# Kernel tuning notes

Measured on AMD Instinct MI355X. Metric: run time of the kernel, lower is better.

The kernel has to match this reference:

```python
import jax, jax.numpy as jnp
import numpy as np


def setup_inputs() -> dict:
    key = jax.random.key(0)
    ks = jax.random.split(key, 24)
    N, C, D_IN, HID, EMB = 8192, 4096, 32, 128, 128
    s = 0.05
    inp = {
        "cand_feat": jax.random.normal(ks[0], (1, C, D_IN), jnp.float32),
        "graph_pos": jax.random.uniform(ks[1], (N, 3), jnp.float32),
        "graph_rad": jax.random.uniform(ks[2], (N,), jnp.float32) + 0.01,
        "L": jnp.ones((1,), jnp.float32),
        "adj": jax.random.uniform(ks[3], (N, N), jnp.float32),
        "mask": jax.random.randint(ks[4], (1, C), 0, 2, jnp.int32),
        # candidate encoder: 32 -> 128 -> 128
        "cW1": jax.random.normal(ks[5], (D_IN, 128), jnp.float32) * s,
        "cb1": jnp.zeros((128,), jnp.float32),
        "cW2": jax.random.normal(ks[6], (128, EMB), jnp.float32) * s,
        "cb2": jnp.zeros((EMB,), jnp.float32),
        # graph encoder input proj: 4 -> 128
        "gW0": jax.random.normal(ks[7], (4, HID), jnp.float32) * s,
        "gb0": jnp.zeros((HID,), jnp.float32),
        # 3 GNN layers: concat(2*HID) -> HID
        "gnnW": jax.random.normal(ks[8], (3, 2 * HID, HID), jnp.float32) * s,
        "gnnb": jnp.zeros((3, HID), jnp.float32),
        # output proj: 2*HID -> EMB
        "goW": jax.random.normal(ks[9], (2 * HID, EMB), jnp.float32) * s,
        "gob": jnp.zeros((EMB,), jnp.float32),
        # fusion: 2*EMB -> 256 -> 128 -> 1
        "fW1": jax.random.normal(ks[10], (2 * EMB, 256), jnp.float32) * s,
        "fb1": jnp.zeros((256,), jnp.float32),
        "fW2": jax.random.normal(ks[11], (256, 128), jnp.float32) * s,
        "fb2": jnp.zeros((128,), jnp.float32),
        "fW3": jax.random.normal(ks[12], (128, 1), jnp.float32) * s,
        "fb3": jnp.zeros((1,), jnp.float32),
    }
    return inp


def reference(cand_feat, graph_pos, graph_rad, L, adj, mask,
              cW1, cb1, cW2, cb2, gW0, gb0, gnnW, gnnb, goW, gob,
              fW1, fb1, fW2, fb2, fW3, fb3):
    relu = jax.nn.relu
    # ---- candidate encoder: [1, C, 32] -> [1, C, 128]
    cand_emb = relu(relu(cand_feat @ cW1 + cb1) @ cW2 + cb2)
    # ---- graph encoder ----
    node = jnp.concatenate([graph_pos / L, (graph_rad / jnp.max(graph_rad))[:, None]], axis=1)  # [N, 4]
    h = relu(node @ gW0 + gb0)  # [N, HID]
    deg = jnp.clip(jnp.sum(adj, axis=-1, keepdims=True), 1.0)  # [N, 1]
    for i in range(gnnW.shape[0]):
        agg = (adj @ h) / deg                       # degree-normalized aggregation
        h = relu(jnp.concatenate([h, agg], axis=-1) @ gnnW[i] + gnnb[i])
    h_glob = jnp.concatenate([jnp.max(h, axis=0), jnp.mean(h, axis=0)], axis=-1)  # [2*HID]
    graph_emb = h_glob @ goW + gob  # [EMB]
    # ---- fusion decoder ----
    g_exp = jnp.broadcast_to(graph_emb[None, None, :], cand_emb.shape)
    combined = jnp.concatenate([cand_emb, g_exp], axis=-1)  # [1, C, 2*EMB]
    scores = (relu(relu(combined @ fW1 + fb1) @ fW2 + fb2) @ fW3 + fb3)[..., 0]  # [1, C]
    return jnp.where(mask == 0, -jnp.inf, scores)
```

## Files before the change

kernel.cpp:

```cpp
#include <hip/hip_runtime.h>
#include <hip/hip_bf16.h>

constexpr int NN  = 8192;
constexpr int CC  = 4096;
constexpr int HD  = 128;
constexpr int KSPLIT = 8;
constexpr int KCHUNK = NN / KSPLIT;
constexpr int NKB = KCHUNK / 32;
constexpr int NK32 = NN / 32;
constexpr int CCH = 32;

typedef __attribute__((ext_vector_type(8))) short bf16x8;
typedef __attribute__((ext_vector_type(4))) float f32x4;

static __device__ __forceinline__ unsigned short f2bf(float f) {
  unsigned int u = __builtin_bit_cast(unsigned int, f);
  unsigned int lsb = (u >> 16) & 1u;
  u += 0x7fffu + lsb;
  return (unsigned short)(u >> 16);
}
static __device__ __forceinline__ float bf2f(unsigned short u) {
  return __builtin_bit_cast(float, ((unsigned int)u) << 16);
}
static __device__ __forceinline__ unsigned long long rfl64(unsigned long long x) {
  unsigned int lo = __builtin_amdgcn_readfirstlane((unsigned int)x);
  unsigned int hi = __builtin_amdgcn_readfirstlane((unsigned int)(x >> 32));
  return ((unsigned long long)hi << 32) | lo;
}

static __device__ __forceinline__ size_t pidx(int t16, int kb, int lane) {
  return (((size_t)t16 * NK32 + kb) * 64 + lane) * 8;
}

__global__ __launch_bounds__(256) void k_radmax(const float* __restrict__ rad, float* out) {
  __shared__ float red[256];
  int t = threadIdx.x;
  float m = 0.0f;
  for (int i = t; i < NN; i += 256) m = fmaxf(m, rad[i]);
  red[t] = m; __syncthreads();
  for (int s = 128; s > 0; s >>= 1) {
    if (t < s) red[t] = fmaxf(red[t], red[t + s]);
    __syncthreads();
  }
  if (t == 0) out[0] = red[0];
}

__global__ __launch_bounds__(256) void k_h0(const float* __restrict__ pos, const float* __restrict__ rad,
                                            const float* __restrict__ Lp, const float* __restrict__ rmax,
                                            const float* __restrict__ gW0, const float* __restrict__ gb0,
                                            float* __restrict__ h, unsigned short* __restrict__ hTP) {
  __shared__ __align__(16) unsigned short lt[128][72];
  int t = threadIdx.x;
  int i0 = blockIdx.x * 64;
  float invL = 1.0f / Lp[0];
  float invR = 1.0f / rmax[0];
  for (int rep = 0; rep < 32; ++rep) {
    int idx = rep * 256 + t;
    int il = idx >> 7, j = idx & 127;
    int i = i0 + il;
    float n0 = pos[i * 3 + 0] * invL, n1 = pos[i * 3 + 1] * invL, n2 = pos[i * 3 + 2] * invL;
    float n3 = rad[i] * invR;
    float v = gb0[j] + n0 * gW0[j] + n1 * gW0[128 + j] + n2 * gW0[256 + j] + n3 * gW0[384 + j];
    v = fmaxf(v, 0.0f);
    h[(size_t)i * HD + j] = v;
    lt[j][il] = f2bf(v);
  }
  __syncthreads();
  #pragma unroll
  for (int it = 0; it < 4; ++it) {
    int idx = it * 256 + t;
    int lane = idx & 63, chunk = idx >> 6;
    int t16 = chunk >> 1, kbL = chunk & 1;
    int j = t16 * 16 + (lane & 15), kg = lane >> 4;
    union { unsigned short v[8]; uint4 q; } pk;
    #pragma unroll
    for (int s = 0; s < 8; ++s) {
      int kp = kg * 4 + (s & 3) + ((s >> 2) * 16);
      pk.v[s] = lt[j][kbL * 32 + kp];
    }
    *(uint4*)(hTP + pidx(t16, blockIdx.x * 2 + kbL, lane)) = pk.q;
  }
}

__global__ __launch_bounds__(256) void k_convP(const float* __restrict__ adj,
                                               unsigned short* __restrict__ adjP,
                                               float* __restrict__ pd) {
  __shared__ __align__(16) unsigned short lt[64 * 256];
  const int t = threadIdx.x;
  const int r0 = blockIdx.x * 64;
  const int c0 = blockIdx.y * 256;
  #pragma unroll
  for (int p = 0; p < 16; ++p) {
    int r = p * 4 + (t >> 6);
    int c = (t & 63) * 4;
    float4 v = *(const float4*)(adj + (size_t)(r0 + r) * NN + c0 + c);
    union { unsigned short u[4]; unsigned long long q; } pk;
    pk.u[0] = f2bf(v.x); pk.u[1] = f2bf(v.y); pk.u[2] = f2bf(v.z); pk.u[3] = f2bf(v.w);
    int g = c >> 3;
    int byte = r * 512 + (((g ^ (r & 7))) << 4) + ((c & 7) * 2);
    *(unsigned long long*)((char*)lt + byte) = pk.q;
  }
  __syncthreads();
  {
    int r = t >> 2, qd = t & 3;
    float s = 0.f;
    #pragma unroll
    for (int k4 = 0; k4 < 16; ++k4) {
      int kk = qd * 64 + k4 * 4;
      int byte = r * 512 + ((((kk >> 3) ^ (r & 7))) << 4) + ((kk & 7) * 2);
      union { unsigned long long q; unsigned short u[4]; } rd;
      rd.q = *(const unsigned long long*)((char*)lt + byte);
      s += bf2f(rd.u[0]) + bf2f(rd.u[1]) + bf2f(rd.u[2]) + bf2f(rd.u[3]);
    }
    s += __shfl_xor(s, 1);
    s += __shfl_xor(s, 2);
    if (qd == 0) pd[(size_t)blockIdx.y * NN + r0 + r] = s;
  }
  const int lane = t & 63, w = t >> 6;
  const int lr = lane & 15, kg = lane >> 4;
  #pragma unroll
  for (int it = 0; it < 8; ++it) {
    int chunk = it * 4 + w;
    int rtl = chunk >> 3, kbL = chunk & 7;
    int r = rtl * 16 + lr;
    union { unsigned short u[8]; uint4 q; } o;
    #pragma unroll
    for (int s = 0; s < 8; ++s) {
      int k = kbL * 32 + kg * 4 + (s & 3) + ((s >> 2) * 16);
      int byte = r * 512 + ((((k >> 3) ^ (r & 7))) << 4) + ((k & 7) * 2);
      o.u[s] = *(const unsigned short*)((char*)lt + byte);
    }
    *(uint4*)(adjP + pidx(blockIdx.x * 4 + rtl, (c0 >> 5) + kbL, lane)) = o.q;
  }
}

__global__ __launch_bounds__(256) void k_degsum(const float* __restrict__ pd, float* __restrict__ deg) {
  int i = blockIdx.x * 256 + threadIdx.x;
  float s = 0.f;
  #pragma unroll
  for (int c = 0; c < CCH; ++c) s += pd[(size_t)c * NN + i];
  deg[i] = fmaxf(s, 1.0f);
}

#define MM16(A_, B_) { _Pragma("unroll")                                  \
    for (int i = 0; i < 4; ++i) {                                         \
      union { uint4 q; bf16x8 v; } ua; ua.q = A_[i];                      \
      _Pragma("unroll")                                                   \
      for (int j = 0; j < 4; ++j) {                                       \
        union { uint4 q; bf16x8 v; } ub; ub.q = B_[j];                    \
        acc[i][j] = __builtin_amdgcn_mfma_f32_16x16x32_bf16(              \
            ua.v, ub.v, acc[i][j], 0, 0, 0);                              \
      } } }

#define GLD(dst, base, imm)                                               \
  asm volatile("global_load_dwordx4 %0, %1, %2 offset:" #imm              \
               : "=v"(dst) : "v"(voff), "s"(base))
#define WAITV(n) do { asm volatile("s_waitcnt vmcnt(" #n ")");            \
                      __builtin_amdgcn_sched_barrier(0); } while (0)

__global__ __launch_bounds__(256) void k_gemmP(const unsigned short* __restrict__ AP,
                                               const unsigned short* __restrict__ hTP,
                                               unsigned short* __restrict__ part) {
  __shared__ __align__(16) char smem[32768];
  const int t = threadIdx.x, lane = t & 63, w = t >> 6;
  const int bm = blockIdx.x, ks = blockIdx.y;
  const int kb0 = ks * NKB;
  const int lr = lane & 15, kg = lane >> 4;
  const int wr = w >> 1, wc = w & 1;
  const unsigned int voff = (unsigned int)(lane * 16);

  unsigned long long bA[4], bB[4];
  #pragma unroll
  for (int q = 0; q < 4; ++q) {
    bA[q] = rfl64((unsigned long long)(AP + pidx(bm * 8 + wr * 4 + q, kb0, 0)));
    bB[q] = rfl64((unsigned long long)(hTP + pidx(wc * 4 + q, kb0, 0)));
  }

  f32x4 acc[4][4];
  #pragma unroll
  for (int i = 0; i < 4; ++i)
    #pragma unroll
    for (int j = 0; j < 4; ++j) acc[i][j] = f32x4{0.f, 0.f, 0.f, 0.f};

  uint4 S0a[4], S0b[4], S1a[4], S1b[4], S2a[4], S2b[4];

  #pragma unroll
  for (int q = 0; q < 4; ++q) { GLD(S0a[q], bA[q], 0); GLD(S0b[q], bB[q], 0); }
  #pragma unroll
  for (int q = 0; q < 4; ++q) { GLD(S1a[q], bA[q], 1024); GLD(S1b[q], bB[q], 1024); }

#define PHASE(CA, CB, NA, NB)                                             \
  do {                                                                    \
    _Pragma("unroll")                                                     \
    for (int q = 0; q < 4; ++q) { GLD(NA[q], bA[q], 2048);                \
                                  GLD(NB[q], bB[q], 2048); }              \
    _Pragma("unroll")                                                     \
    for (int q = 0; q < 4; ++q) { bA[q] += 1024; bB[q] += 1024; }         \
    WAITV(16);                                                            \
    MM16(CA, CB);                                                         \
    __builtin_amdgcn_sched_barrier(0);                                    \
  } while (0)

  for (int r = 0; r < 10; ++r) {
    PHASE(S0a, S0b, S2a, S2b);
    PHASE(S1a, S1b, S0a, S0b);
    PHASE(S2a, S2b, S1a, S1b);
  }
  WAITV(8);
  MM16(S0a, S0b);
  __builtin_amdgcn_sched_barrier(0);
  WAITV(0);
  MM16(S1a, S1b);
#undef PHASE

  __syncthreads();
  unsigned short* pl = (unsigned short*)smem;
  #pragma unroll
  for (int i = 0; i < 4; ++i)
    #pragma unroll
    for (int j = 0; j < 4; ++j)
      #pragma unroll
      for (int jj = 0; jj < 4; ++jj)
        pl[(wr * 64 + i * 16 + kg * 4 + jj) * 128 + wc * 64 + j * 16 + lr] =
            f2bf(acc[i][j][jj]);
  __syncthreads();
  uint4* gout = (uint4*)(part + (size_t)ks * NN * HD + (size_t)bm * 128 * HD);
  const uint4* ls = (const uint4*)smem;
  #pragma unroll
  for (int k = 0; k < 8; ++k) gout[k * 256 + t] = ls[k * 256 + t];
}

__global__ __launch_bounds__(256) void k_update(const unsigned short* __restrict__ part,
                                                const float* __restrict__ deg,
                                                const float* __restrict__ hin,
                                                const float* __restrict__ W, const float* __restrict__ bias,
                                                float* __restrict__ hout, unsigned short* __restrict__ hTP,
                                                int last) {
  __shared__ float cc[16][256];
  __shared__ __align__(16) unsigned short lt2[128][20];
  int t = threadIdx.x;
  int r0 = blockIdx.x * 16;
  for (int rep = 0; rep < 8; ++rep) {
    int idx = rep * 256 + t;
    int rl = idx >> 7, j = idx & 127;
    int row = r0 + rl;
    float s = 0.f;
    for (int ks = 0; ks < KSPLIT; ++ks)
      s += bf2f(part[((size_t)ks * NN + row) * HD + j]);
    cc[rl][128 + j] = s / deg[row];
    cc[rl][j] = hin[(size_t)row * HD + j];
  }
  __syncthreads();
  int jo = t & 127, rbase = t >> 7;
  float accv[8];
  float bj = bias[jo];
  for (int rr = 0; rr < 8; ++rr) accv[rr] = bj;
  for (int jj = 0; jj < 256; ++jj) {
    float wv = W[jj * HD + jo];
    for (int rr = 0; rr < 8; ++rr) accv[rr] += cc[rbase + rr * 2][jj] * wv;
  }
  for (int rr = 0; rr < 8; ++rr) {
    int rl = rbase + rr * 2;
    float v = fmaxf(accv[rr], 0.f);
    hout[(size_t)(r0 + rl) * HD + jo] = v;
    if (!last) lt2[jo][rl] = f2bf(v);
  }
  if (!last) {
    __syncthreads();
    const int p = (r0 >> 4) & 1;
    const int kb = r0 >> 5;
    #pragma unroll
    for (int it = 0; it < 2; ++it) {
      int idx = it * 256 + t;
      int lane = idx & 63, t16 = idx >> 6;
      int j = t16 * 16 + (lane & 15), kg = lane >> 4;
      union { unsigned short v[4]; uint2 q; } pk;
      #pragma unroll
      for (int d = 0; d < 4; ++d) pk.v[d] = lt2[j][kg * 4 + d];
      *(uint2*)(hTP + pidx(t16, kb, lane) + p * 4) = pk.q;
    }
  }
}

__global__ __launch_bounds__(256) void k_pool(const float* __restrict__ h,
                                              float* __restrict__ pmax, float* __restrict__ psum) {
  int b = blockIdx.x, t = threadIdx.x;
  int j = t & 127, half = t >> 7;
  int r0 = b * 128 + half * 64;
  float mx = -1e30f, sm = 0.f;
  for (int r = r0; r < r0 + 64; ++r) {
    float v = h[(size_t)r * HD + j];
    mx = fmaxf(mx, v); sm += v;
  }
  __shared__ float lm[2][128], ls[2][128];
  lm[half][j] = mx; ls[half][j] = sm;
  __syncthreads();
  if (half == 0) {
    pmax[b * 128 + j] = fmaxf(lm[0][j], lm[1][j]);
    psum[b * 128 + j] = ls[0][j] + ls[1][j];
  }
}

__global__ __launch_bounds__(256) void k_glob(const float* __restrict__ pmax, const float* __restrict__ psum,
                                              const float* __restrict__ goW, const float* __restrict__ gob,
                                              float* __restrict__ ge) {
  __shared__ float hg[256];
  int t = threadIdx.x;
  int j = t & 127, which = t >> 7;
  if (which == 0) {
    float m = -1e30f;
    for (int b = 0; b < 64; ++b) m = fmaxf(m, pmax[b * 128 + j]);
    hg[j] = m;
  } else {
    float s = 0.f;
    for (int b = 0; b < 64; ++b) s += psum[b * 128 + j];
    hg[128 + j] = s * (1.0f / (float)NN);
  }
  __syncthreads();
  if (t < 128) {
    float s = gob[t];
    for (int jj = 0; jj < 256; ++jj) s += hg[jj] * goW[jj * HD + t];
    ge[t] = s;
  }
}

__global__ __launch_bounds__(256) void k_fusion(const float* __restrict__ cand, const float* __restrict__ ge,
                                                const int* __restrict__ mask,
                                                const float* __restrict__ cW1, const float* __restrict__ cb1,
                                                const float* __restrict__ cW2, const float* __restrict__ cb2,
                                                const float* __restrict__ fW1, const float* __restrict__ fb1,
                                                const float* __restrict__ fW2, const float* __restrict__ fb2,
                                                const float* __restrict__ fW3, const float* __restrict__ fb3,
                                                float* __restrict__ out) {
  __shared__ float x[16][32];
  __shared__ float t1[16][128];
  __shared__ float t2[16][128];
  __shared__ float u1[16][256];
  __shared__ float u2[16][129];
  __shared__ float geL[128];
  int t = threadIdx.x;
  int c0 = blockIdx.x * 16;
  if (t < 128) geL[t] = ge[t];
  for (int rep = 0; rep < 2; ++rep) {
    int idx = rep * 256 + t;
    int cl = idx >> 5, d = idx & 31;
    x[cl][d] = cand[(size_t)(c0 + cl) * 32 + d];
  }
  __syncthreads();
  {
    int j = t & 127, cg = (t >> 7) * 8;
    float a[8]; float bj = cb1[j];
    for (int q = 0; q < 8; ++q) a[q] = bj;
    for (int d = 0; d < 32; ++d) {
      float wv = cW1[d * 128 + j];
      for (int q = 0; q < 8; ++q) a[q] += x[cg + q][d] * wv;
    }
    for (int q = 0; q < 8; ++q) t1[cg + q][j] = fmaxf(a[q], 0.f);
  }
  __syncthreads();
  {
    int j = t & 127, cg = (t >> 7) * 8;
    float a[8]; float bj = cb2[j];
    for (int q = 0; q < 8; ++q) a[q] = bj;
    for (int d = 0; d < 128; ++d) {
      float wv = cW2[d * 128 + j];
      for (int q = 0; q < 8; ++q) a[q] += t1[cg + q][d] * wv;
    }
    for (int q = 0; q < 8; ++q) t2[cg + q][j] = fmaxf(a[q], 0.f);
  }
  __syncthreads();
  {
    int jo = t;
    float gp = fb1[jo];
    for (int d = 0; d < 128; ++d) gp += geL[d] * fW1[(128 + d) * 256 + jo];
    float a[16];
    for (int q = 0; q < 16; ++q) a[q] = gp;
    for (int d = 0; d < 128; ++d) {
      float wv = fW1[d * 256 + jo];
      for (int q = 0; q < 16; ++q) a[q] += t2[q][d] * wv;
    }
    for (int q = 0; q < 16; ++q) u1[q][jo] = fmaxf(a[q], 0.f);
  }
  __syncthreads();
  {
    int j = t & 127, cg = (t >> 7) * 8;
    float a[8]; float bj = fb2[j];
    for (int q = 0; q < 8; ++q) a[q] = bj;
    for (int d = 0; d < 256; ++d) {
      float wv = fW2[d * 128 + j];
      for (int q = 0; q < 8; ++q) a[q] += u1[cg + q][d] * wv;
    }
    for (int q = 0; q < 8; ++q) u2[cg + q][j] = fmaxf(a[q], 0.f);
  }
  __syncthreads();
  if (t < 16) {
    int c = c0 + t;
    float s = fb3[0];
    for (int d = 0; d < 128; ++d) s += u2[t][d] * fW3[d];
    out[c] = (mask[c] == 0) ? -3.0e38f : s;
  }
}

extern "C" void kernel_launch(void* const* d_in, const int* in_sizes, int n_in,
                              void* d_out, int out_size, void* d_ws, size_t ws_size,
                              hipStream_t stream) {
  const float* cand = (const float*)d_in[0];
  const float* pos  = (const float*)d_in[1];
  const float* rad  = (const float*)d_in[2];
  const float* Lp   = (const float*)d_in[3];
  const float* adj  = (const float*)d_in[4];
  const int*   mask = (const int*)d_in[5];
  const float* cW1 = (const float*)d_in[6];
  const float* cb1 = (const float*)d_in[7];
  const float* cW2 = (const float*)d_in[8];
  const float* cb2 = (const float*)d_in[9];
  const float* gW0 = (const float*)d_in[10];
  const float* gb0 = (const float*)d_in[11];
  const float* gnnW = (const float*)d_in[12];
  const float* gnnb = (const float*)d_in[13];
  const float* goW = (const float*)d_in[14];
  const float* gob = (const float*)d_in[15];
  const float* fW1 = (const float*)d_in[16];
  const float* fb1 = (const float*)d_in[17];
  const float* fW2 = (const float*)d_in[18];
  const float* fb2 = (const float*)d_in[19];
  const float* fW3 = (const float*)d_in[20];
  const float* fb3 = (const float*)d_in[21];

  char* ws = (char*)d_ws;
  float* h            = (float*)ws;
  unsigned short* hTP = (unsigned short*)(ws + (4ull << 20));
  float* rmax         = (float*)(ws + (6ull << 20));
  float* pmax         = (float*)(ws + (6ull << 20) + 4096);
  float* psum         = pmax + 64 * 128;
  float* ge           = psum + 64 * 128;
  float* deg          = (float*)(ws + (6ull << 20) + (128u << 10));
  float* pd           = (float*)(ws + (7ull << 20));
  unsigned short* part = (unsigned short*)(ws + (8ull << 20));
  unsigned short* adjP = (unsigned short*)(ws + (25ull << 20));

  k_radmax<<<1, 256, 0, stream>>>(rad, rmax);
  k_h0<<<NN / 64, 256, 0, stream>>>(pos, rad, Lp, rmax, gW0, gb0, h, hTP);
  {
    dim3 gc(NN / 64, CCH);
    k_convP<<<gc, 256, 0, stream>>>(adj, adjP, pd);
  }
  k_degsum<<<NN / 256, 256, 0, stream>>>(pd, deg);

  dim3 g(NN / 128, KSPLIT);
  for (int l = 0; l < 3; ++l) {
    k_gemmP<<<g, 256, 0, stream>>>(adjP, hTP, part);
    k_update<<<NN / 16, 256, 0, stream>>>(part, deg, h,
                                          gnnW + l * 256 * HD, gnnb + l * HD, h, hTP, l == 2);
  }
  k_pool<<<64, 256, 0, stream>>>(h, pmax, psum);
  k_glob<<<1, 256, 0, stream>>>(pmax, psum, goW, gob, ge);
  k_fusion<<<CC / 16, 256, 0, stream>>>(cand, ge, mask, cW1, cb1, cW2, cb2,
                                        fW1, fb1, fW2, fb2, fW3, fb3, (float*)d_out);
}
```

Before: 401.0 us.

## Quantize adjacency and node features to fp8 and use fp8 MFMA aggregation

```diff
diff --git a/kernel.cpp b/kernel.cpp
--- a/kernel.cpp
+++ b/kernel.cpp
@@ -6,11 +6,10 @@
 constexpr int HD  = 128;
 constexpr int KSPLIT = 8;
 constexpr int KCHUNK = NN / KSPLIT;
-constexpr int NKB = KCHUNK / 32;
-constexpr int NK32 = NN / 32;
+constexpr int NKP_CHUNK = KCHUNK / 64;
+constexpr int NKP_TOT = NN / 64;
 constexpr int CCH = 32;
 
-typedef __attribute__((ext_vector_type(8))) short bf16x8;
 typedef __attribute__((ext_vector_type(4))) float f32x4;
 
 static __device__ __forceinline__ unsigned short f2bf(float f) {
@@ -22,14 +21,19 @@
 static __device__ __forceinline__ float bf2f(unsigned short u) {
   return __builtin_bit_cast(float, ((unsigned int)u) << 16);
 }
+static __device__ __forceinline__ float e4m3f(unsigned char b) {
+  unsigned e = (b >> 3) & 0xF, m = b & 7;
+  if (e) return __builtin_bit_cast(float, ((e + 120u) << 23) | (m << 20));
+  return (float)m * 0.001953125f;
+}
 static __device__ __forceinline__ unsigned long long rfl64(unsigned long long x) {
   unsigned int lo = __builtin_amdgcn_readfirstlane((unsigned int)x);
   unsigned int hi = __builtin_amdgcn_readfirstlane((unsigned int)(x >> 32));
   return ((unsigned long long)hi << 32) | lo;
 }
 
-static __device__ __forceinline__ size_t pidx(int t16, int kb, int lane) {
-  return (((size_t)t16 * NK32 + kb) * 64 + lane) * 8;
+static __device__ __forceinline__ size_t pidx8(int t16, int kbp, int lane) {
+  return (((size_t)t16 * NKP_TOT + kbp) * 64 + lane) * 16;
 }
 
 __global__ __launch_bounds__(256) void k_radmax(const float* __restrict__ rad, float* out) {
@@ -48,8 +52,8 @@
 __global__ __launch_bounds__(256) void k_h0(const float* __restrict__ pos, const float* __restrict__ rad,
                                             const float* __restrict__ Lp, const float* __restrict__ rmax,
                                             const float* __restrict__ gW0, const float* __restrict__ gb0,
-                                            float* __restrict__ h, unsigned short* __restrict__ hTP) {
-  __shared__ __align__(16) unsigned short lt[128][72];
+                                            float* __restrict__ h, unsigned char* __restrict__ h8) {
+  __shared__ __align__(8) unsigned char lt8[128][80];
   int t = threadIdx.x;
   int i0 = blockIdx.x * 64;
   float invL = 1.0f / Lp[0];
@@ -63,74 +67,73 @@
     float v = gb0[j] + n0 * gW0[j] + n1 * gW0[128 + j] + n2 * gW0[256 + j] + n3 * gW0[384 + j];
     v = fmaxf(v, 0.0f);
     h[(size_t)i * HD + j] = v;
-    lt[j][il] = f2bf(v);
-  }
-  __syncthreads();
-  #pragma unroll
-  for (int it = 0; it < 4; ++it) {
-    int idx = it * 256 + t;
-    int lane = idx & 63, chunk = idx >> 6;
-    int t16 = chunk >> 1, kbL = chunk & 1;
-    int j = t16 * 16 + (lane & 15), kg = lane >> 4;
-    union { unsigned short v[8]; uint4 q; } pk;
-    #pragma unroll
-    for (int s = 0; s < 8; ++s) {
-      int kp = kg * 4 + (s & 3) + ((s >> 2) * 16);
-      pk.v[s] = lt[j][kbL * 32 + kp];
-    }
-    *(uint4*)(hTP + pidx(t16, blockIdx.x * 2 + kbL, lane)) = pk.q;
-  }
-}
-
-__global__ __launch_bounds__(256) void k_convP(const float* __restrict__ adj,
-                                               unsigned short* __restrict__ adjP,
-                                               float* __restrict__ pd) {
-  __shared__ __align__(16) unsigned short lt[64 * 256];
+    int enc = __builtin_amdgcn_cvt_pk_fp8_f32(v, 0.0f, 0, false);
+    lt8[j][il] = (unsigned char)(enc & 0xFF);
+  }
+  __syncthreads();
+  const int lane = t & 63, w = t >> 6;
+  #pragma unroll
+  for (int it = 0; it < 2; ++it) {
+    int t16 = it * 4 + w;
+    int j = t16 * 16 + (lane & 15);
+    int ib = (lane >> 4) * 8;
+    unsigned long long lo = *(const unsigned long long*)(&lt8[j][ib]);
+    unsigned long long hi = *(const unsigned long long*)(&lt8[j][ib + 32]);
+    uint4 q;
+    q.x = (unsigned)lo; q.y = (unsigned)(lo >> 32);
+    q.z = (unsigned)hi; q.w = (unsigned)(hi >> 32);
+    *(uint4*)(h8 + pidx8(t16, blockIdx.x, lane)) = q;
+  }
+}
+
+__global__ __launch_bounds__(256) void k_convP8(const float* __restrict__ adj,
+                                                unsigned char* __restrict__ adjP8,
+                                                float* __restrict__ pd) {
+  __shared__ __align__(8) unsigned char lt[64 * 256];
   const int t = threadIdx.x;
   const int r0 = blockIdx.x * 64;
   const int c0 = blockIdx.y * 256;
+  const int l = t & 63, w = t >> 6;
   #pragma unroll
   for (int p = 0; p < 16; ++p) {
-    int r = p * 4 + (t >> 6);
-    int c = (t & 63) * 4;
+    int r = p * 4 + w;
+    int c = l * 4;
     float4 v = *(const float4*)(adj + (size_t)(r0 + r) * NN + c0 + c);
-    union { unsigned short u[4]; unsigned long long q; } pk;
-    pk.u[0] = f2bf(v.x); pk.u[1] = f2bf(v.y); pk.u[2] = f2bf(v.z); pk.u[3] = f2bf(v.w);
-    int g = c >> 3;
-    int byte = r * 512 + (((g ^ (r & 7))) << 4) + ((c & 7) * 2);
-    *(unsigned long long*)((char*)lt + byte) = pk.q;
+    int b32 = __builtin_amdgcn_cvt_pk_fp8_f32(v.x, v.y, 0, false);
+    b32 = __builtin_amdgcn_cvt_pk_fp8_f32(v.z, v.w, b32, true);
+    int g = l >> 1;
+    int addr = r * 256 + ((g ^ (r & 7)) << 3) + ((l & 1) * 4);
+    *(unsigned int*)(lt + addr) = (unsigned int)b32;
   }
   __syncthreads();
   {
     int r = t >> 2, qd = t & 3;
     float s = 0.f;
     #pragma unroll
-    for (int k4 = 0; k4 < 16; ++k4) {
-      int kk = qd * 64 + k4 * 4;
-      int byte = r * 512 + ((((kk >> 3) ^ (r & 7))) << 4) + ((kk & 7) * 2);
-      union { unsigned long long q; unsigned short u[4]; } rd;
-      rd.q = *(const unsigned long long*)((char*)lt + byte);
-      s += bf2f(rd.u[0]) + bf2f(rd.u[1]) + bf2f(rd.u[2]) + bf2f(rd.u[3]);
+    for (int k8 = 0; k8 < 8; ++k8) {
+      int g = qd * 8 + k8;
+      int addr = r * 256 + ((g ^ (r & 7)) << 3);
+      unsigned long long v = *(const unsigned long long*)(lt + addr);
+      #pragma unroll
+      for (int b = 0; b < 8; ++b) s += e4m3f((unsigned char)(v >> (b * 8)));
     }
     s += __shfl_xor(s, 1);
     s += __shfl_xor(s, 2);
     if (qd == 0) pd[(size_t)blockIdx.y * NN + r0 + r] = s;
   }
-  const int lane = t & 63, w = t >> 6;
-  const int lr = lane & 15, kg = lane >> 4;
-  #pragma unroll
-  for (int it = 0; it < 8; ++it) {
+  #pragma unroll
+  for (int it = 0; it < 4; ++it) {
     int chunk = it * 4 + w;
-    int rtl = chunk >> 3, kbL = chunk & 7;
-    int r = rtl * 16 + lr;
-    union { unsigned short u[8]; uint4 q; } o;
-    #pragma unroll
-    for (int s = 0; s < 8; ++s) {
-      int k = kbL * 32 + kg * 4 + (s & 3) + ((s >> 2) * 16);
-      int byte = r * 512 + ((((k >> 3) ^ (r & 7))) << 4) + ((k & 7) * 2);
-      o.u[s] = *(const unsigned short*)((char*)lt + byte);
-    }
-    *(uint4*)(adjP + pidx(blockIdx.x * 4 + rtl, (c0 >> 5) + kbL, lane)) = o.q;
+    int t16l = chunk >> 2, kbpl = chunk & 3;
+    int r = t16l * 16 + (l & 15);
+    int cb0 = kbpl * 64 + (l >> 4) * 8;
+    int g0 = cb0 >> 3, g1 = g0 + 4;
+    unsigned long long lo = *(const unsigned long long*)(lt + r * 256 + ((g0 ^ (r & 7)) << 3));
+    unsigned long long hi = *(const unsigned long long*)(lt + r * 256 + ((g1 ^ (r & 7)) << 3));
+    uint4 q;
+    q.x = (unsigned)lo; q.y = (unsigned)(lo >> 32);
+    q.z = (unsigned)hi; q.w = (unsigned)(hi >> 32);
+    *(uint4*)(adjP8 + pidx8(blockIdx.x * 4 + t16l, (c0 >> 6) + kbpl, l)) = q;
   }
 }
 
@@ -142,15 +145,25 @@
   deg[i] = fmaxf(s, 1.0f);
 }
 
-#define MM16(A_, B_) { _Pragma("unroll")                                  \
-    for (int i = 0; i < 4; ++i) {                                         \
-      union { uint4 q; bf16x8 v; } ua; ua.q = A_[i];                      \
-      _Pragma("unroll")                                                   \
-      for (int j = 0; j < 4; ++j) {                                       \
-        union { uint4 q; bf16x8 v; } ub; ub.q = B_[j];                    \
-        acc[i][j] = __builtin_amdgcn_mfma_f32_16x16x32_bf16(              \
-            ua.v, ub.v, acc[i][j], 0, 0, 0);                              \
-      } } }
+#define MM32(SA_, SB_) {                                                    \
+  _Pragma("unroll")                                                         \
+  for (int i = 0; i < 4; ++i) {                                             \
+    union { uint4 q; long long ll[2]; } ua; ua.q = SA_[i];                  \
+    _Pragma("unroll")                                                       \
+    for (int j = 0; j < 4; ++j) {                                           \
+      union { uint4 q; long long ll[2]; } ub; ub.q = SB_[j];                \
+      acc[i][j] = __builtin_amdgcn_mfma_f32_16x16x32_fp8_fp8(               \
+          ua.ll[0], ub.ll[0], acc[i][j], 0, 0, 0);                          \
+    } }                                                                     \
+  _Pragma("unroll")                                                         \
+  for (int i = 0; i < 4; ++i) {                                             \
+    union { uint4 q; long long ll[2]; } ua; ua.q = SA_[i];                  \
+    _Pragma("unroll")                                                       \
+    for (int j = 0; j < 4; ++j) {                                           \
+      union { uint4 q; long long ll[2]; } ub; ub.q = SB_[j];                \
+      acc[i][j] = __builtin_amdgcn_mfma_f32_16x16x32_fp8_fp8(               \
+          ua.ll[1], ub.ll[1], acc[i][j], 0, 0, 0);                          \
+    } } }
 
 #define GLD(dst, base, imm)                                               \
   asm volatile("global_load_dwordx4 %0, %1, %2 offset:" #imm              \
@@ -158,13 +171,13 @@
 #define WAITV(n) do { asm volatile("s_waitcnt vmcnt(" #n ")");            \
                       __builtin_amdgcn_sched_barrier(0); } while (0)
 
-__global__ __launch_bounds__(256) void k_gemmP(const unsigned short* __restrict__ AP,
-                                               const unsigned short* __restrict__ hTP,
+__global__ __launch_bounds__(256) void k_gemmP(const unsigned char* __restrict__ AP,
+                                               const unsigned char* __restrict__ h8,
                                                unsigned short* __restrict__ part) {
   __shared__ __align__(16) char smem[32768];
   const int t = threadIdx.x, lane = t & 63, w = t >> 6;
   const int bm = blockIdx.x, ks = blockIdx.y;
-  const int kb0 = ks * NKB;
+  const int kb0p = ks * NKP_CHUNK;
   const int lr = lane & 15, kg = lane >> 4;
   const int wr = w >> 1, wc = w & 1;
   const unsigned int voff = (unsigned int)(lane * 16);
@@ -172,8 +185,8 @@
   unsigned long long bA[4], bB[4];
   #pragma unroll
   for (int q = 0; q < 4; ++q) {
-    bA[q] = rfl64((unsigned long long)(AP + pidx(bm * 8 + wr * 4 + q, kb0, 0)));
-    bB[q] = rfl64((unsigned long long)(hTP + pidx(wc * 4 + q, kb0, 0)));
+    bA[q] = rfl64((unsigned long long)(AP + pidx8(bm * 8 + wr * 4 + q, kb0p, 0)));
+    bB[q] = rfl64((unsigned long long)(h8 + pidx8(wc * 4 + q, kb0p, 0)));
   }
 
   f32x4 acc[4][4];
@@ -197,20 +210,22 @@
     _Pragma("unroll")                                                     \
     for (int q = 0; q < 4; ++q) { bA[q] += 1024; bB[q] += 1024; }         \
     WAITV(16);                                                            \
-    MM16(CA, CB);                                                         \
+    MM32(CA, CB);                                                         \
     __builtin_amdgcn_sched_barrier(0);                                    \
   } while (0)
 
-  for (int r = 0; r < 10; ++r) {
+  for (int r = 0; r < 4; ++r) {
     PHASE(S0a, S0b, S2a, S2b);
     PHASE(S1a, S1b, S0a, S0b);
     PHASE(S2a, S2b, S1a, S1b);
   }
+  PHASE(S0a, S0b, S2a, S2b);
+  PHASE(S1a, S1b, S0a, S0b);
   WAITV(8);
-  MM16(S0a, S0b);
+  MM32(S2a, S2b);
   __builtin_amdgcn_sched_barrier(0);
   WAITV(0);
-  MM16(S1a, S1b);
+  MM32(S0a, S0b);
 #undef PHASE
 
   __syncthreads();
@@ -234,10 +249,10 @@
                                                 const float* __restrict__ deg,
                                                 const float* __restrict__ hin,
                                                 const float* __restrict__ W, const float* __restrict__ bias,
-                                                float* __restrict__ hout, unsigned short* __restrict__ hTP,
+                                                float* __restrict__ hout, unsigned char* __restrict__ h8,
                                                 int last) {
   __shared__ float cc[16][256];
-  __shared__ __align__(16) unsigned short lt2[128][20];
+  __shared__ __align__(8) unsigned char lt2[128][24];
   int t = threadIdx.x;
   int r0 = blockIdx.x * 16;
   for (int rep = 0; rep < 8; ++rep) {
@@ -263,21 +278,25 @@
     int rl = rbase + rr * 2;
     float v = fmaxf(accv[rr], 0.f);
     hout[(size_t)(r0 + rl) * HD + jo] = v;
-    if (!last) lt2[jo][rl] = f2bf(v);
+    if (!last) {
+      int enc = __builtin_amdgcn_cvt_pk_fp8_f32(v, 0.0f, 0, false);
+      lt2[jo][rl] = (unsigned char)(enc & 0xFF);
+    }
   }
   if (!last) {
     __syncthreads();
-    const int p = (r0 >> 4) & 1;
-    const int kb = r0 >> 5;
+    const int q = (r0 >> 4) & 3;
+    const int kbp = r0 >> 6;
     #pragma unroll
     for (int it = 0; it < 2; ++it) {
       int idx = it * 256 + t;
-      int lane = idx & 63, t16 = idx >> 6;
-      int j = t16 * 16 + (lane & 15), kg = lane >> 4;
-      union { unsigned short v[4]; uint2 q; } pk;
-      #pragma unroll
-      for (int d = 0; d < 4; ++d) pk.v[d] = lt2[j][kg * 4 + d];
-      *(uint2*)(hTP + pidx(t16, kb, lane) + p * 4) = pk.q;
+      int lane = idx & 63, t16 = (it * 256 + t) >> 6;
+      int g = lane >> 4;
+      if ((g >> 1) == (q & 1)) {
+        int j = t16 * 16 + (lane & 15);
+        unsigned long long v = *(const unsigned long long*)(&lt2[j][(g & 1) * 8]);
+        *(unsigned long long*)(h8 + pidx8(t16, kbp, lane) + (q >> 1) * 8) = v;
+      }
     }
   }
 }
@@ -429,7 +448,7 @@
 
   char* ws = (char*)d_ws;
   float* h            = (float*)ws;
-  unsigned short* hTP = (unsigned short*)(ws + (4ull << 20));
+  unsigned char* h8   = (unsigned char*)(ws + (4ull << 20));
   float* rmax         = (float*)(ws + (6ull << 20));
   float* pmax         = (float*)(ws + (6ull << 20) + 4096);
   float* psum         = pmax + 64 * 128;
@@ -437,21 +456,21 @@
   float* deg          = (float*)(ws + (6ull << 20) + (128u << 10));
   float* pd           = (float*)(ws + (7ull << 20));
   unsigned short* part = (unsigned short*)(ws + (8ull << 20));
-  unsigned short* adjP = (unsigned short*)(ws + (25ull << 20));
+  unsigned char* adjP8 = (unsigned char*)(ws + (25ull << 20));
 
   k_radmax<<<1, 256, 0, stream>>>(rad, rmax);
-  k_h0<<<NN / 64, 256, 0, stream>>>(pos, rad, Lp, rmax, gW0, gb0, h, hTP);
+  k_h0<<<NN / 64, 256, 0, stream>>>(pos, rad, Lp, rmax, gW0, gb0, h, h8);
   {
     dim3 gc(NN / 64, CCH);
-    k_convP<<<gc, 256, 0, stream>>>(adj, adjP, pd);
+    k_convP8<<<gc, 256, 0, stream>>>(adj, adjP8, pd);
   }
   k_degsum<<<NN / 256, 256, 0, stream>>>(pd, deg);
 
   dim3 g(NN / 128, KSPLIT);
   for (int l = 0; l < 3; ++l) {
-    k_gemmP<<<g, 256, 0, stream>>>(adjP, hTP, part);
+    k_gemmP<<<g, 256, 0, stream>>>(adjP8, h8, part);
     k_update<<<NN / 16, 256, 0, stream>>>(part, deg, h,
-                                          gnnW + l * 256 * HD, gnnb + l * HD, h, hTP, l == 2);
+                                          gnnW + l * 256 * HD, gnnb + l * HD, h, h8, l == 2);
   }
   k_pool<<<64, 256, 0, stream>>>(h, pmax, psum);
   k_glob<<<1, 256, 0, stream>>>(pmax, psum, goW, gob, ge);
```

Measured after the change: 354.1 us. -11.7%, faster.
